# Kernel tuning notes

Measured on AMD Instinct MI355X. Metric: run time of the kernel, lower is better.

The kernel has to match this reference:

```python
import jax, jax.numpy as jnp
import numpy as np

N_LOC, C, A, H, X, STEPS = 500000, 128, 24, 256, 128, 4


def setup_inputs() -> dict:
    key = jax.random.key(0)
    ks = jax.random.split(key, 12)
    def rn(i, shape, scale=0.05):
        return jax.random.normal(ks[i], shape, dtype=jnp.float32) * scale
    return {
        "x": jax.random.normal(ks[0], (1, X), dtype=jnp.float32),
        "h0": jnp.zeros((1, H), jnp.float32),
        "memory_contents": rn(1, (N_LOC, C), 0.01),
        "memory_addresses": rn(2, (N_LOC, A), 0.1),
        "W_query": rn(3, (H, A + C)),
        "b_query": jnp.zeros((A + C,), jnp.float32),
        "u_sharpen": rn(4, (H,)),
        "b_sharpen": jnp.zeros((1,), jnp.float32),
        "W_erase": rn(5, (H, C)),
        "b_erase": jnp.zeros((C,), jnp.float32),
        "W_cand_h": rn(6, (H, C)),
        "W_cand_x": rn(7, (X, C)),
        "b_cand": jnp.zeros((C,), jnp.float32),
        "W_ih": rn(8, (X + C, 3 * H)),
        "W_hh": rn(9, (H, 3 * H)),
        "b_ih": jnp.zeros((3 * H,), jnp.float32),
        "b_hh": jnp.zeros((3 * H,), jnp.float32),
        "num_addressing_steps": STEPS,
    }


def _gru_cell(inp, h, W_ih, W_hh, b_ih, b_hh):
    # torch.nn.GRUCell semantics
    gi = inp @ W_ih + b_ih  # (1, 3H)
    gh = h @ W_hh + b_hh    # (1, 3H)
    i_r, i_z, i_n = jnp.split(gi, 3, axis=-1)
    h_r, h_z, h_n = jnp.split(gh, 3, axis=-1)
    r = jax.nn.sigmoid(i_r + h_r)
    z = jax.nn.sigmoid(i_z + h_z)
    n = jnp.tanh(i_n + r * h_n)
    return (1.0 - z) * n + z * h


def reference(x, h0, memory_contents, memory_addresses, W_query, b_query,
              u_sharpen, b_sharpen, W_erase, b_erase, W_cand_h, W_cand_x,
              b_cand, W_ih, W_hh, b_ih, b_hh, num_addressing_steps):
    h = h0                      # (1, H)
    mem = memory_contents       # (N, C)
    for _ in range(num_addressing_steps):
        # --- content-based addressing over full memory [addresses || contents] ---
        q = h @ W_query + b_query                              # (1, A+C)
        beta = jax.nn.softplus(h @ u_sharpen + b_sharpen) + 1.0  # (1,)
        sim = memory_addresses @ q[0, :A] + mem @ q[0, A:]     # (N,)
        w = jax.nn.softmax(beta[0] * sim)                      # (N,)
        # --- read ---
        content = (w @ mem)[None, :]                           # (1, C)
        # --- controller step ---
        h = _gru_cell(jnp.concatenate([x, content], axis=1), h, W_ih, W_hh, b_ih, b_hh)
        # --- write: erase + candidate ---
        erase = jax.nn.sigmoid(h @ W_erase + b_erase)          # (1, C)
        cand = jax.nn.relu(h @ W_cand_h + x @ W_cand_x + b_cand)  # (1, C)
        mem = mem * (1.0 - w[:, None] * erase) + w[:, None] * cand
    return h
```

## Files before the change

kernel.cpp:

```cpp
#include <hip/hip_runtime.h>
#include <hip/hip_bf16.h>

#define N_LOC 500000
#define C 128
#define A 24
#define AC 152
#define H 256
#define X 128
#define G3 768
#define GRID_BIG 1024

typedef unsigned short ushort_t;

__device__ __forceinline__ float sigmoidf_(float x) { return 1.0f / (1.0f + __expf(-x)); }

__device__ __forceinline__ ushort_t f2bf(float f) {
    unsigned u = __float_as_uint(f);
    u += 0x7FFFu + ((u >> 16) & 1u);
    return (ushort_t)(u >> 16);
}
__device__ __forceinline__ float bf2f(ushort_t s) {
    return __uint_as_float(((unsigned)s) << 16);
}

template <int NPREV, bool WRITE_E, bool CONVERT>
__global__ __launch_bounds__(256) void big_pass(
    const float* __restrict__ mem0, const float* __restrict__ addr,
    ushort_t* __restrict__ membf, ushort_t* __restrict__ addrbf,
    const float* __restrict__ qacc,
    const float* __restrict__ ehist,
    const float* __restrict__ chist,
    const float* __restrict__ ssum4,
    const float* __restrict__ earr,
    float* __restrict__ enew,
    float* __restrict__ part)
{
    const int lane = threadIdx.x & 31;
    const int rg   = threadIdx.x >> 5;

    const float4 qc = *(const float4*)(qacc + A + 4 * lane);
    float4 qa = make_float4(0.f, 0.f, 0.f, 0.f);
    if (lane < 6) qa = *(const float4*)(qacc + 4 * lane);
    float beta;
    { float t = qacc[AC]; beta = (t > 20.f ? t : log1pf(__expf(t))) + 1.0f; }

    constexpr int NP = (NPREV > 0) ? NPREV : 1;
    float4 er[NP], cd[NP];
    float inv_s[NP];
#pragma unroll
    for (int s = 0; s < NPREV; ++s) {
        float4 et = *(const float4*)(ehist + (s + 1) * C + 4 * lane);
        er[s].x = sigmoidf_(et.x); er[s].y = sigmoidf_(et.y);
        er[s].z = sigmoidf_(et.z); er[s].w = sigmoidf_(et.w);
        float4 ct = *(const float4*)(chist + (s + 1) * C + 4 * lane);
        cd[s].x = fmaxf(ct.x, 0.f); cd[s].y = fmaxf(ct.y, 0.f);
        cd[s].z = fmaxf(ct.z, 0.f); cd[s].w = fmaxf(ct.w, 0.f);
        inv_s[s] = 1.0f / ssum4[s + 1];
    }

    float4 acc = make_float4(0.f, 0.f, 0.f, 0.f);
    float sumloc = 0.f;
    const int stride = gridDim.x * 8;

    for (int i = blockIdx.x * 8 + rg; i < N_LOC; i += stride) {
        float4 m, a4 = make_float4(0.f, 0.f, 0.f, 0.f);
        if (CONVERT) {
            m = *(const float4*)(mem0 + (size_t)i * C + 4 * lane);
            ushort4 mu; mu.x = f2bf(m.x); mu.y = f2bf(m.y);
            mu.z = f2bf(m.z); mu.w = f2bf(m.w);
            *(ushort4*)(membf + (size_t)i * C + 4 * lane) = mu;
            if (lane < 6) {
                a4 = *(const float4*)(addr + (size_t)i * A + 4 * lane);
                ushort4 au; au.x = f2bf(a4.x); au.y = f2bf(a4.y);
                au.z = f2bf(a4.z); au.w = f2bf(a4.w);
                *(ushort4*)(addrbf + (size_t)i * A + 4 * lane) = au;
            }
        } else {
            ushort4 mu = *(const ushort4*)(membf + (size_t)i * C + 4 * lane);
            m = make_float4(bf2f(mu.x), bf2f(mu.y), bf2f(mu.z), bf2f(mu.w));
            if (lane < 6) {
                ushort4 au = *(const ushort4*)(addrbf + (size_t)i * A + 4 * lane);
                a4 = make_float4(bf2f(au.x), bf2f(au.y), bf2f(au.z), bf2f(au.w));
            }
        }

#pragma unroll
        for (int s = 0; s < NPREV; ++s) {
            float w = earr[s * N_LOC + i] * inv_s[s];
            m.x = m.x * (1.f - w * er[s].x) + w * cd[s].x;
            m.y = m.y * (1.f - w * er[s].y) + w * cd[s].y;
            m.z = m.z * (1.f - w * er[s].z) + w * cd[s].z;
            m.w = m.w * (1.f - w * er[s].w) + w * cd[s].w;
        }

        float s = m.x * qc.x + m.y * qc.y + m.z * qc.z + m.w * qc.w;
        s += a4.x * qa.x + a4.y * qa.y + a4.z * qa.z + a4.w * qa.w;
        s += __shfl_xor(s, 1);
        s += __shfl_xor(s, 2);
        s += __shfl_xor(s, 4);
        s += __shfl_xor(s, 8);
        s += __shfl_xor(s, 16);
        float ev = __expf(beta * s);
        if (WRITE_E && lane == 0) enew[i] = ev;
        if (lane == 0) sumloc += ev;
        acc.x += ev * m.x; acc.y += ev * m.y;
        acc.z += ev * m.z; acc.w += ev * m.w;
    }

    __shared__ float sc[8][C];
    __shared__ float ssum[256];
    *(float4*)(&sc[rg][4 * lane]) = acc;
    ssum[threadIdx.x] = sumloc;
    __syncthreads();
    if (threadIdx.x < C) {
        float v = 0.f;
#pragma unroll
        for (int g = 0; g < 8; ++g) v += sc[g][threadIdx.x];
        part[blockIdx.x * 132 + threadIdx.x] = v;
    }
    for (int off = 128; off > 0; off >>= 1) {
        if (threadIdx.x < off) ssum[threadIdx.x] += ssum[threadIdx.x + off];
        __syncthreads();
    }
    if (threadIdx.x == 0) part[blockIdx.x * 132 + C] = ssum[0];
}

__global__ __launch_bounds__(256) void reduce_part(
    const float* __restrict__ part, float* __restrict__ craw,
    float* __restrict__ ssum4, int step)
{
    const int j = blockIdx.x;
    float v = 0.f;
    for (int b = threadIdx.x; b < GRID_BIG; b += 256)
        v += part[b * 132 + j];
    __shared__ float sh[256];
    sh[threadIdx.x] = v;
    __syncthreads();
    for (int off = 128; off > 0; off >>= 1) {
        if (threadIdx.x < off) sh[threadIdx.x] += sh[threadIdx.x + off];
        __syncthreads();
    }
    if (threadIdx.x == 0) {
        craw[j] = sh[0];
        if (j == C) ssum4[step] = sh[0];
    }
}

__global__ __launch_bounds__(256) void prex(
    const float* __restrict__ x, const float* __restrict__ W_ih,
    const float* __restrict__ b_ih, const float* __restrict__ W_cx,
    float* __restrict__ gix, float* __restrict__ candx)
{
    const int tid = threadIdx.x;
    float a0 = 0.f, a1 = 0.f, a2 = 0.f, ac = 0.f;
    const int k0 = blockIdx.x * 8;
    for (int k = k0; k < k0 + 8; ++k) {
        float xk = x[k];
        const float* row = W_ih + (size_t)k * G3;
        a0 += xk * row[tid];
        a1 += xk * row[256 + tid];
        a2 += xk * row[512 + tid];
        if (tid < C) ac += xk * W_cx[k * C + tid];
    }
    const bool b0 = (blockIdx.x == 0);
    atomicAdd(gix + tid,        a0 + (b0 ? b_ih[tid] : 0.f));
    atomicAdd(gix + 256 + tid,  a1 + (b0 ? b_ih[256 + tid] : 0.f));
    atomicAdd(gix + 512 + tid,  a2 + (b0 ? b_ih[512 + tid] : 0.f));
    if (tid < C) atomicAdd(candx + tid, ac);
}

__global__ __launch_bounds__(256) void post(
    const float* __restrict__ h,
    const float* __restrict__ W_er, const float* __restrict__ b_er,
    const float* __restrict__ W_ch, const float* __restrict__ b_cd,
    const float* __restrict__ W_q,  const float* __restrict__ b_q,
    const float* __restrict__ u_sh, const float* __restrict__ b_sh,
    const float* __restrict__ candx,
    float* __restrict__ eslot, float* __restrict__ cslot,
    float* __restrict__ qacc)
{
    const int tid = threadIdx.x;
    float ae = 0.f, ac = 0.f, aq = 0.f, ab = 0.f;
    const int k0 = blockIdx.x * 16;
    for (int k = k0; k < k0 + 16; ++k) {
        float hk = h[k];
        if (tid < C)  { ae += hk * W_er[k * C + tid]; ac += hk * W_ch[k * C + tid]; }
        if (tid < AC)   aq += hk * W_q[k * AC + tid];
        if (tid == 255) ab += hk * u_sh[k];
    }
    const bool b0 = (blockIdx.x == 0);
    if (tid < C) {
        atomicAdd(eslot + tid, ae + (b0 ? b_er[tid] : 0.f));
        atomicAdd(cslot + tid, ac + (b0 ? (candx[tid] + b_cd[tid]) : 0.f));
    }
    if (tid < AC)   atomicAdd(qacc + tid, aq + (b0 ? b_q[tid] : 0.f));
    if (tid == 255) atomicAdd(qacc + AC, ab + (b0 ? b_sh[0] : 0.f));
}

__global__ __launch_bounds__(256) void gatesfin(
    const float* __restrict__ craw, const float* __restrict__ hprev,
    const float* __restrict__ W_ih, const float* __restrict__ W_hh,
    const float* __restrict__ b_hh, const float* __restrict__ gix,
    float* __restrict__ p2, float* __restrict__ hout,
    float* __restrict__ qacc, unsigned* __restrict__ counter)
{
    const int tid = threadIdx.x;
    const float inv = 1.0f / craw[C];
    float gi0 = 0.f, gi1 = 0.f, gi2 = 0.f, gh0 = 0.f, gh1 = 0.f, gh2 = 0.f;
    const int kc0 = blockIdx.x * 8;
    for (int k = kc0; k < kc0 + 8; ++k) {
        float ck = craw[k] * inv;
        const float* row = W_ih + (size_t)(X + k) * G3;
        gi0 += ck * row[tid]; gi1 += ck * row[256 + tid]; gi2 += ck * row[512 + tid];
    }
    const int kh0 = blockIdx.x * 16;
    for (int k = kh0; k < kh0 + 16; ++k) {
        float hk = hprev[k];
        const float* row = W_hh + (size_t)k * G3;
        gh0 += hk * row[tid]; gh1 += hk * row[256 + tid]; gh2 += hk * row[512 + tid];
    }
    const bool b0 = (blockIdx.x == 0);
    float* pb = p2 + blockIdx.x * 1536;
    pb[tid]        = gi0 + (b0 ? gix[tid] : 0.f);
    pb[256 + tid]  = gi1 + (b0 ? gix[256 + tid] : 0.f);
    pb[512 + tid]  = gi2 + (b0 ? gix[512 + tid] : 0.f);
    pb[768 + tid]  = gh0 + (b0 ? b_hh[tid] : 0.f);
    pb[1024 + tid] = gh1 + (b0 ? b_hh[256 + tid] : 0.f);
    pb[1280 + tid] = gh2 + (b0 ? b_hh[512 + tid] : 0.f);
    __threadfence();
    __syncthreads();
    __shared__ int lastBlk;
    if (tid == 0) lastBlk = (atomicAdd(counter, 1u) == 15u) ? 1 : 0;
    __syncthreads();
    if (!lastBlk) return;
    __threadfence();
    float ir = 0.f, iz = 0.f, in_ = 0.f, hr = 0.f, hz = 0.f, hn = 0.f;
    for (int b = 0; b < 16; ++b) {
        const float* q = p2 + b * 1536;
        ir += q[tid]; iz += q[256 + tid]; in_ += q[512 + tid];
        hr += q[768 + tid]; hz += q[1024 + tid]; hn += q[1280 + tid];
    }
    float r = sigmoidf_(ir + hr);
    float z = sigmoidf_(iz + hz);
    float n = tanhf(in_ + r * hn);
    hout[tid] = (1.f - z) * n + z * hprev[tid];
    if (tid < 160) qacc[tid] = 0.f;
    if (tid == 0) *counter = 0u;
}

extern "C" void kernel_launch(void* const* d_in, const int* in_sizes, int n_in,
                              void* d_out, int out_size, void* d_ws, size_t ws_size,
                              hipStream_t stream) {
    (void)in_sizes; (void)n_in; (void)out_size; (void)ws_size;
    const float* x    = (const float*)d_in[0];
    const float* h0   = (const float*)d_in[1];
    const float* mem0 = (const float*)d_in[2];
    const float* addr = (const float*)d_in[3];
    const float* W_q  = (const float*)d_in[4];
    const float* b_q  = (const float*)d_in[5];
    const float* u_sh = (const float*)d_in[6];
    const float* b_sh = (const float*)d_in[7];
    const float* W_er = (const float*)d_in[8];
    const float* b_er = (const float*)d_in[9];
    const float* W_ch = (const float*)d_in[10];
    const float* W_cx = (const float*)d_in[11];
    const float* b_cd = (const float*)d_in[12];
    const float* W_ih = (const float*)d_in[13];
    const float* W_hh = (const float*)d_in[14];
    const float* b_ih = (const float*)d_in[15];
    const float* b_hh = (const float*)d_in[16];
    float* hout = (float*)d_out;

    float*    e      = (float*)d_ws;
    ushort_t* membf  = (ushort_t*)(e + 3 * N_LOC);
    ushort_t* addrbf = membf + (size_t)N_LOC * C;
    float*    part   = (float*)(addrbf + (size_t)N_LOC * A);
    float*    S      = part + GRID_BIG * 132;
    float*    craw   = S;
    float*    qacc   = S + 144;
    float*    ehist  = S + 304;
    float*    chist  = S + 816;
    float*    gix    = S + 1328;
    float*    candx  = S + 2096;
    float*    ssum4  = S + 2224;
    unsigned* counter= (unsigned*)(S + 2232);
    float*    p2     = S + 2240;

    hipMemsetAsync(S, 0, 2240 * sizeof(float), stream);
    prex<<<16, 256, 0, stream>>>(x, W_ih, b_ih, W_cx, gix, candx);
    post<<<16, 256, 0, stream>>>(h0, W_er, b_er, W_ch, b_cd, W_q, b_q, u_sh, b_sh,
                                 candx, ehist, chist, qacc);
    big_pass<0, true, true><<<GRID_BIG, 256, 0, stream>>>(
        mem0, addr, membf, addrbf, qacc, ehist, chist, ssum4, e, e, part);
    reduce_part<<<129, 256, 0, stream>>>(part, craw, ssum4, 1);
    gatesfin<<<16, 256, 0, stream>>>(craw, h0, W_ih, W_hh, b_hh, gix, p2, hout,
                                     qacc, counter);
    post<<<16, 256, 0, stream>>>(hout, W_er, b_er, W_ch, b_cd, W_q, b_q, u_sh, b_sh,
                                 candx, ehist + C, chist + C, qacc);
    big_pass<1, true, false><<<GRID_BIG, 256, 0, stream>>>(
        mem0, addr, membf, addrbf, qacc, ehist, chist, ssum4, e, e + N_LOC, part);
    reduce_part<<<129, 256, 0, stream>>>(part, craw, ssum4, 2);
    gatesfin<<<16, 256, 0, stream>>>(craw, hout, W_ih, W_hh, b_hh, gix, p2, hout,
                                     qacc, counter);
    post<<<16, 256, 0, stream>>>(hout, W_er, b_er, W_ch, b_cd, W_q, b_q, u_sh, b_sh,
                                 candx, ehist + 2 * C, chist + 2 * C, qacc);
    big_pass<2, true, false><<<GRID_BIG, 256, 0, stream>>>(
        mem0, addr, membf, addrbf, qacc, ehist, chist, ssum4, e, e + 2 * N_LOC, part);
    reduce_part<<<129, 256, 0, stream>>>(part, craw, ssum4, 3);
    gatesfin<<<16, 256, 0, stream>>>(craw, hout, W_ih, W_hh, b_hh, gix, p2, hout,
                                     qacc, counter);
    post<<<16, 256, 0, stream>>>(hout, W_er, b_er, W_ch, b_cd, W_q, b_q, u_sh, b_sh,
                                 candx, ehist + 3 * C, chist + 3 * C, qacc);
    big_pass<3, false, false><<<GRID_BIG, 256, 0, stream>>>(
        mem0, addr, membf, addrbf, qacc, ehist, chist, ssum4, e, e, part);
    reduce_part<<<129, 256, 0, stream>>>(part, craw, ssum4, 4);
    gatesfin<<<16, 256, 0, stream>>>(craw, hout, W_ih, W_hh, b_hh, gix, p2, hout,
                                     qacc, counter);
}
```

Baseline: 749.1 us.

## Store memory snapshot in scaled FP8 and fuse step reduction, gates, and projections

The bf16 copy of the memory contents becomes an FP8 (e4m3) copy scaled by 64, with the scale folded into the query and candidate vectors. This halves the bytes each big pass reads per row. Separately, the reduce, gates and post kernels merge into one step_fin kernel using a transposed partial-sum layout, and prex plus the first post merge into init_k, which cuts kernel launches per step. The cost is much coarser precision for memory values, since FP8 keeps only three mantissa bits, which may break tolerance. The last block now also does the full 256-wide H projection serially.

```diff
diff --git a/kernel.cpp b/kernel.cpp
--- a/kernel.cpp
+++ b/kernel.cpp
@@ -1,5 +1,4 @@
 #include <hip/hip_runtime.h>
-#include <hip/hip_bf16.h>
 
 #define N_LOC 500000
 #define C 128
@@ -9,8 +8,12 @@
 #define X 128
 #define G3 768
 #define GRID_BIG 1024
+#define MSCALE 64.0f
+#define MINV 0.015625f
 
 typedef unsigned short ushort_t;
+typedef unsigned char uchar_t;
+typedef float floatx2 __attribute__((ext_vector_type(2)));
 
 __device__ __forceinline__ float sigmoidf_(float x) { return 1.0f / (1.0f + __expf(-x)); }
 
@@ -23,10 +26,60 @@
     return __uint_as_float(((unsigned)s) << 16);
 }
 
+#if defined(__has_builtin)
+#if __has_builtin(__builtin_amdgcn_cvt_pk_fp8_f32) && __has_builtin(__builtin_amdgcn_cvt_pk_f32_fp8)
+#define HAVE_HW_FP8 1
+#endif
+#endif
+
+__device__ __forceinline__ unsigned f2fp8_sw(float f) {
+    unsigned sgn = (__float_as_uint(f) >> 24) & 0x80u;
+    float af = fminf(fabsf(f), 448.0f);
+    unsigned q;
+    if (af < 0.015625f) {
+        q = (unsigned)__float2int_rn(af * 512.0f);
+    } else {
+        unsigned a = __float_as_uint(af);
+        a += 0x7FFFFu + ((a >> 20) & 1u);
+        unsigned e = (a >> 23) - 120u;
+        q = (e << 3) | ((a >> 20) & 7u);
+        if (q > 126u) q = 126u;
+    }
+    return q | sgn;
+}
+__device__ __forceinline__ float fp8d_sw(unsigned b) {
+    unsigned sgn = (b & 0x80u) << 24;
+    unsigned e = (b >> 3) & 15u;
+    unsigned m = b & 7u;
+    float fn = __uint_as_float(sgn | ((e + 120u) << 23) | (m << 20));
+    float fd = __uint_as_float(sgn | __float_as_uint((float)m * 0.001953125f));
+    return e ? fn : fd;
+}
+__device__ __forceinline__ unsigned pack_fp8x4(float4 m) {
+#ifdef HAVE_HW_FP8
+    int w = 0;
+    w = __builtin_amdgcn_cvt_pk_fp8_f32(m.x, m.y, w, false);
+    w = __builtin_amdgcn_cvt_pk_fp8_f32(m.z, m.w, w, true);
+    return (unsigned)w;
+#else
+    return f2fp8_sw(m.x) | (f2fp8_sw(m.y) << 8) | (f2fp8_sw(m.z) << 16) | (f2fp8_sw(m.w) << 24);
+#endif
+}
+__device__ __forceinline__ float4 unpack_fp8x4(unsigned w) {
+#ifdef HAVE_HW_FP8
+    floatx2 lo = __builtin_amdgcn_cvt_pk_f32_fp8((int)w, false);
+    floatx2 hi = __builtin_amdgcn_cvt_pk_f32_fp8((int)w, true);
+    return make_float4(lo[0], lo[1], hi[0], hi[1]);
+#else
+    return make_float4(fp8d_sw(w & 255u), fp8d_sw((w >> 8) & 255u),
+                       fp8d_sw((w >> 16) & 255u), fp8d_sw(w >> 24));
+#endif
+}
+
 template <int NPREV, bool WRITE_E, bool CONVERT>
 __global__ __launch_bounds__(256) void big_pass(
     const float* __restrict__ mem0, const float* __restrict__ addr,
-    ushort_t* __restrict__ membf, ushort_t* __restrict__ addrbf,
+    uchar_t* __restrict__ memq, ushort_t* __restrict__ addrbf,
     const float* __restrict__ qacc,
     const float* __restrict__ ehist,
     const float* __restrict__ chist,
@@ -38,7 +91,8 @@
     const int lane = threadIdx.x & 31;
     const int rg   = threadIdx.x >> 5;
 
-    const float4 qc = *(const float4*)(qacc + A + 4 * lane);
+    float4 qc = *(const float4*)(qacc + A + 4 * lane);
+    qc.x *= MINV; qc.y *= MINV; qc.z *= MINV; qc.w *= MINV;
     float4 qa = make_float4(0.f, 0.f, 0.f, 0.f);
     if (lane < 6) qa = *(const float4*)(qacc + 4 * lane);
     float beta;
@@ -53,8 +107,10 @@
         er[s].x = sigmoidf_(et.x); er[s].y = sigmoidf_(et.y);
         er[s].z = sigmoidf_(et.z); er[s].w = sigmoidf_(et.w);
         float4 ct = *(const float4*)(chist + (s + 1) * C + 4 * lane);
-        cd[s].x = fmaxf(ct.x, 0.f); cd[s].y = fmaxf(ct.y, 0.f);
-        cd[s].z = fmaxf(ct.z, 0.f); cd[s].w = fmaxf(ct.w, 0.f);
+        cd[s].x = fmaxf(ct.x, 0.f) * MSCALE;
+        cd[s].y = fmaxf(ct.y, 0.f) * MSCALE;
+        cd[s].z = fmaxf(ct.z, 0.f) * MSCALE;
+        cd[s].w = fmaxf(ct.w, 0.f) * MSCALE;
         inv_s[s] = 1.0f / ssum4[s + 1];
     }
 
@@ -65,10 +121,10 @@
     for (int i = blockIdx.x * 8 + rg; i < N_LOC; i += stride) {
         float4 m, a4 = make_float4(0.f, 0.f, 0.f, 0.f);
         if (CONVERT) {
-            m = *(const float4*)(mem0 + (size_t)i * C + 4 * lane);
-            ushort4 mu; mu.x = f2bf(m.x); mu.y = f2bf(m.y);
-            mu.z = f2bf(m.z); mu.w = f2bf(m.w);
-            *(ushort4*)(membf + (size_t)i * C + 4 * lane) = mu;
+            float4 mf = *(const float4*)(mem0 + (size_t)i * C + 4 * lane);
+            m.x = mf.x * MSCALE; m.y = mf.y * MSCALE;
+            m.z = mf.z * MSCALE; m.w = mf.w * MSCALE;
+            *(unsigned*)(memq + (size_t)i * C + 4 * lane) = pack_fp8x4(m);
             if (lane < 6) {
                 a4 = *(const float4*)(addr + (size_t)i * A + 4 * lane);
                 ushort4 au; au.x = f2bf(a4.x); au.y = f2bf(a4.y);
@@ -76,8 +132,8 @@
                 *(ushort4*)(addrbf + (size_t)i * A + 4 * lane) = au;
             }
         } else {
-            ushort4 mu = *(const ushort4*)(membf + (size_t)i * C + 4 * lane);
-            m = make_float4(bf2f(mu.x), bf2f(mu.y), bf2f(mu.z), bf2f(mu.w));
+            unsigned mw = *(const unsigned*)(memq + (size_t)i * C + 4 * lane);
+            m = unpack_fp8x4(mw);
             if (lane < 6) {
                 ushort4 au = *(const ushort4*)(addrbf + (size_t)i * A + 4 * lane);
                 a4 = make_float4(bf2f(au.x), bf2f(au.y), bf2f(au.z), bf2f(au.w));
@@ -93,14 +149,14 @@
             m.w = m.w * (1.f - w * er[s].w) + w * cd[s].w;
         }
 
-        float s = m.x * qc.x + m.y * qc.y + m.z * qc.z + m.w * qc.w;
-        s += a4.x * qa.x + a4.y * qa.y + a4.z * qa.z + a4.w * qa.w;
-        s += __shfl_xor(s, 1);
-        s += __shfl_xor(s, 2);
-        s += __shfl_xor(s, 4);
-        s += __shfl_xor(s, 8);
-        s += __shfl_xor(s, 16);
-        float ev = __expf(beta * s);
+        float sv = m.x * qc.x + m.y * qc.y + m.z * qc.z + m.w * qc.w;
+        sv += a4.x * qa.x + a4.y * qa.y + a4.z * qa.z + a4.w * qa.w;
+        sv += __shfl_xor(sv, 1);
+        sv += __shfl_xor(sv, 2);
+        sv += __shfl_xor(sv, 4);
+        sv += __shfl_xor(sv, 8);
+        sv += __shfl_xor(sv, 16);
+        float ev = __expf(beta * sv);
         if (WRITE_E && lane == 0) enew[i] = ev;
         if (lane == 0) sumloc += ev;
         acc.x += ev * m.x; acc.y += ev * m.y;
@@ -116,117 +172,122 @@
         float v = 0.f;
 #pragma unroll
         for (int g = 0; g < 8; ++g) v += sc[g][threadIdx.x];
-        part[blockIdx.x * 132 + threadIdx.x] = v;
+        part[(size_t)threadIdx.x * GRID_BIG + blockIdx.x] = v;
     }
     for (int off = 128; off > 0; off >>= 1) {
         if (threadIdx.x < off) ssum[threadIdx.x] += ssum[threadIdx.x + off];
         __syncthreads();
     }
-    if (threadIdx.x == 0) part[blockIdx.x * 132 + C] = ssum[0];
-}
-
-__global__ __launch_bounds__(256) void reduce_part(
-    const float* __restrict__ part, float* __restrict__ craw,
-    float* __restrict__ ssum4, int step)
-{
-    const int j = blockIdx.x;
-    float v = 0.f;
-    for (int b = threadIdx.x; b < GRID_BIG; b += 256)
-        v += part[b * 132 + j];
-    __shared__ float sh[256];
-    sh[threadIdx.x] = v;
-    __syncthreads();
-    for (int off = 128; off > 0; off >>= 1) {
-        if (threadIdx.x < off) sh[threadIdx.x] += sh[threadIdx.x + off];
-        __syncthreads();
-    }
-    if (threadIdx.x == 0) {
-        craw[j] = sh[0];
-        if (j == C) ssum4[step] = sh[0];
-    }
-}
-
-__global__ __launch_bounds__(256) void prex(
-    const float* __restrict__ x, const float* __restrict__ W_ih,
-    const float* __restrict__ b_ih, const float* __restrict__ W_cx,
-    float* __restrict__ gix, float* __restrict__ candx)
+    if (threadIdx.x == 0) part[(size_t)C * GRID_BIG + blockIdx.x] = ssum[0];
+}
+
+__global__ __launch_bounds__(256) void init_k(
+    const float* __restrict__ x, const float* __restrict__ h0,
+    const float* __restrict__ W_ih, const float* __restrict__ b_ih,
+    const float* __restrict__ W_cx,
+    const float* __restrict__ W_er, const float* __restrict__ b_er,
+    const float* __restrict__ W_ch, const float* __restrict__ b_cd,
+    const float* __restrict__ W_q,  const float* __restrict__ b_q,
+    const float* __restrict__ u_sh, const float* __restrict__ b_sh,
+    float* __restrict__ gix, float* __restrict__ candx,
+    float* __restrict__ eslot, float* __restrict__ cslot,
+    float* __restrict__ qacc)
 {
     const int tid = threadIdx.x;
-    float a0 = 0.f, a1 = 0.f, a2 = 0.f, ac = 0.f;
-    const int k0 = blockIdx.x * 8;
-    for (int k = k0; k < k0 + 8; ++k) {
-        float xk = x[k];
-        const float* row = W_ih + (size_t)k * G3;
-        a0 += xk * row[tid];
-        a1 += xk * row[256 + tid];
-        a2 += xk * row[512 + tid];
-        if (tid < C) ac += xk * W_cx[k * C + tid];
-    }
     const bool b0 = (blockIdx.x == 0);
-    atomicAdd(gix + tid,        a0 + (b0 ? b_ih[tid] : 0.f));
-    atomicAdd(gix + 256 + tid,  a1 + (b0 ? b_ih[256 + tid] : 0.f));
-    atomicAdd(gix + 512 + tid,  a2 + (b0 ? b_ih[512 + tid] : 0.f));
-    if (tid < C) atomicAdd(candx + tid, ac);
-}
-
-__global__ __launch_bounds__(256) void post(
-    const float* __restrict__ h,
+    {
+        float a0 = 0.f, a1 = 0.f, a2 = 0.f, ac = 0.f;
+        const int k0 = blockIdx.x * 8;
+        for (int k = k0; k < k0 + 8; ++k) {
+            float xk = x[k];
+            const float* row = W_ih + (size_t)k * G3;
+            a0 += xk * row[tid];
+            a1 += xk * row[256 + tid];
+            a2 += xk * row[512 + tid];
+            if (tid < C) ac += xk * W_cx[k * C + tid];
+        }
+        atomicAdd(gix + tid,        a0 + (b0 ? b_ih[tid] : 0.f));
+        atomicAdd(gix + 256 + tid,  a1 + (b0 ? b_ih[256 + tid] : 0.f));
+        atomicAdd(gix + 512 + tid,  a2 + (b0 ? b_ih[512 + tid] : 0.f));
+        if (tid < C) atomicAdd(candx + tid, ac);
+    }
+    {
+        float ae = 0.f, ac2 = 0.f, aq = 0.f, ab = 0.f;
+        const int k0 = blockIdx.x * 16;
+        for (int k = k0; k < k0 + 16; ++k) {
+            float hk = h0[k];
+            if (tid < C)  { ae += hk * W_er[k * C + tid]; ac2 += hk * W_ch[k * C + tid]; }
+            if (tid < AC)   aq += hk * W_q[k * AC + tid];
+            if (tid == 255) ab += hk * u_sh[k];
+        }
+        if (tid < C) {
+            atomicAdd(eslot + tid, ae + (b0 ? b_er[tid] : 0.f));
+            atomicAdd(cslot + tid, ac2 + (b0 ? b_cd[tid] : 0.f));
+        }
+        if (tid < AC)   atomicAdd(qacc + tid, aq + (b0 ? b_q[tid] : 0.f));
+        if (tid == 255) atomicAdd(qacc + AC, ab + (b0 ? b_sh[0] : 0.f));
+    }
+}
+
+__global__ __launch_bounds__(256) void step_fin(
+    const float* __restrict__ part, float* __restrict__ craw,
+    float* __restrict__ ssum4, int step,
+    const float* __restrict__ hprev,
+    const float* __restrict__ W_ih, const float* __restrict__ W_hh,
+    const float* __restrict__ b_hh, const float* __restrict__ gix,
+    float* __restrict__ p2, float* __restrict__ hout,
     const float* __restrict__ W_er, const float* __restrict__ b_er,
     const float* __restrict__ W_ch, const float* __restrict__ b_cd,
     const float* __restrict__ W_q,  const float* __restrict__ b_q,
     const float* __restrict__ u_sh, const float* __restrict__ b_sh,
     const float* __restrict__ candx,
     float* __restrict__ eslot, float* __restrict__ cslot,
-    float* __restrict__ qacc)
+    float* __restrict__ qnext,
+    unsigned* __restrict__ counter, int do_post)
 {
     const int tid = threadIdx.x;
-    float ae = 0.f, ac = 0.f, aq = 0.f, ab = 0.f;
-    const int k0 = blockIdx.x * 16;
-    for (int k = k0; k < k0 + 16; ++k) {
-        float hk = h[k];
-        if (tid < C)  { ae += hk * W_er[k * C + tid]; ac += hk * W_ch[k * C + tid]; }
-        if (tid < AC)   aq += hk * W_q[k * AC + tid];
-        if (tid == 255) ab += hk * u_sh[k];
-    }
-    const bool b0 = (blockIdx.x == 0);
-    if (tid < C) {
-        atomicAdd(eslot + tid, ae + (b0 ? b_er[tid] : 0.f));
-        atomicAdd(cslot + tid, ac + (b0 ? (candx[tid] + b_cd[tid]) : 0.f));
-    }
-    if (tid < AC)   atomicAdd(qacc + tid, aq + (b0 ? b_q[tid] : 0.f));
-    if (tid == 255) atomicAdd(qacc + AC, ab + (b0 ? b_sh[0] : 0.f));
-}
-
-__global__ __launch_bounds__(256) void gatesfin(
-    const float* __restrict__ craw, const float* __restrict__ hprev,
-    const float* __restrict__ W_ih, const float* __restrict__ W_hh,
-    const float* __restrict__ b_hh, const float* __restrict__ gix,
-    float* __restrict__ p2, float* __restrict__ hout,
-    float* __restrict__ qacc, unsigned* __restrict__ counter)
-{
-    const int tid = threadIdx.x;
-    const float inv = 1.0f / craw[C];
-    float gi0 = 0.f, gi1 = 0.f, gi2 = 0.f, gh0 = 0.f, gh1 = 0.f, gh2 = 0.f;
-    const int kc0 = blockIdx.x * 8;
-    for (int k = kc0; k < kc0 + 8; ++k) {
-        float ck = craw[k] * inv;
-        const float* row = W_ih + (size_t)(X + k) * G3;
-        gi0 += ck * row[tid]; gi1 += ck * row[256 + tid]; gi2 += ck * row[512 + tid];
-    }
-    const int kh0 = blockIdx.x * 16;
-    for (int k = kh0; k < kh0 + 16; ++k) {
-        float hk = hprev[k];
-        const float* row = W_hh + (size_t)k * G3;
-        gh0 += hk * row[tid]; gh1 += hk * row[256 + tid]; gh2 += hk * row[512 + tid];
-    }
-    const bool b0 = (blockIdx.x == 0);
-    float* pb = p2 + blockIdx.x * 1536;
-    pb[tid]        = gi0 + (b0 ? gix[tid] : 0.f);
-    pb[256 + tid]  = gi1 + (b0 ? gix[256 + tid] : 0.f);
-    pb[512 + tid]  = gi2 + (b0 ? gix[512 + tid] : 0.f);
-    pb[768 + tid]  = gh0 + (b0 ? b_hh[tid] : 0.f);
-    pb[1024 + tid] = gh1 + (b0 ? b_hh[256 + tid] : 0.f);
-    pb[1280 + tid] = gh2 + (b0 ? b_hh[512 + tid] : 0.f);
+    __shared__ float scol[4];
+    __shared__ float myc[9];
+
+    for (int j = blockIdx.x; j < C + 1; j += 16) {
+        float v = 0.f;
+        for (int b = tid; b < GRID_BIG; b += 256) v += part[(size_t)j * GRID_BIG + b];
+        v += __shfl_xor(v, 1);  v += __shfl_xor(v, 2);  v += __shfl_xor(v, 4);
+        v += __shfl_xor(v, 8);  v += __shfl_xor(v, 16); v += __shfl_xor(v, 32);
+        if ((tid & 63) == 0) scol[tid >> 6] = v;
+        __syncthreads();
+        if (tid == 0) {
+            float sv = scol[0] + scol[1] + scol[2] + scol[3];
+            if (j < C) myc[(j - blockIdx.x) >> 4] = sv * MINV;
+            else       { craw[C] = sv; ssum4[step] = sv; }
+        }
+        __syncthreads();
+    }
+
+    {
+        float gi0 = 0.f, gi1 = 0.f, gi2 = 0.f;
+        int idx = 0;
+        for (int j = blockIdx.x; j < C; j += 16, ++idx) {
+            float ck = myc[idx];
+            const float* row = W_ih + (size_t)(X + j) * G3;
+            gi0 += ck * row[tid]; gi1 += ck * row[256 + tid]; gi2 += ck * row[512 + tid];
+        }
+        float gh0 = 0.f, gh1 = 0.f, gh2 = 0.f;
+        const int kh0 = blockIdx.x * 16;
+        for (int k = kh0; k < kh0 + 16; ++k) {
+            float hk = hprev[k];
+            const float* row = W_hh + (size_t)k * G3;
+            gh0 += hk * row[tid]; gh1 += hk * row[256 + tid]; gh2 += hk * row[512 + tid];
+        }
+        float* pb = p2 + blockIdx.x * 1536;
+        pb[tid]        = gi0;
+        pb[256 + tid]  = gi1;
+        pb[512 + tid]  = gi2;
+        pb[768 + tid]  = gh0;
+        pb[1024 + tid] = gh1;
+        pb[1280 + tid] = gh2;
+    }
+
     __threadfence();
     __syncthreads();
     __shared__ int lastBlk;
@@ -234,18 +295,43 @@
     __syncthreads();
     if (!lastBlk) return;
     __threadfence();
-    float ir = 0.f, iz = 0.f, in_ = 0.f, hr = 0.f, hz = 0.f, hn = 0.f;
+
+    float giA = 0.f, giB = 0.f, giC = 0.f, ghA = 0.f, ghB = 0.f, ghC = 0.f;
     for (int b = 0; b < 16; ++b) {
         const float* q = p2 + b * 1536;
-        ir += q[tid]; iz += q[256 + tid]; in_ += q[512 + tid];
-        hr += q[768 + tid]; hz += q[1024 + tid]; hn += q[1280 + tid];
-    }
+        giA += q[tid];       giB += q[256 + tid];  giC += q[512 + tid];
+        ghA += q[768 + tid]; ghB += q[1024 + tid]; ghC += q[1280 + tid];
+    }
+    const float inv = 1.0f / craw[C];
+    float ir  = giA * inv + gix[tid];
+    float iz  = giB * inv + gix[256 + tid];
+    float in_ = giC * inv + gix[512 + tid];
+    float hr  = ghA + b_hh[tid];
+    float hz  = ghB + b_hh[256 + tid];
+    float hn  = ghC + b_hh[512 + tid];
     float r = sigmoidf_(ir + hr);
     float z = sigmoidf_(iz + hz);
     float n = tanhf(in_ + r * hn);
-    hout[tid] = (1.f - z) * n + z * hprev[tid];
-    if (tid < 160) qacc[tid] = 0.f;
-    if (tid == 0) *counter = 0u;
+    float h = (1.f - z) * n + z * hprev[tid];
+    hout[tid] = h;
+    if (!do_post) return;
+
+    __shared__ float hsh[H];
+    hsh[tid] = h;
+    __syncthreads();
+    float ae = 0.f, ac = 0.f, aq = 0.f, ab = 0.f;
+    for (int k = 0; k < H; ++k) {
+        float hk = hsh[k];
+        if (tid < C)  { ae += hk * W_er[k * C + tid]; ac += hk * W_ch[k * C + tid]; }
+        if (tid < AC)   aq += hk * W_q[k * AC + tid];
+        if (tid == 255) ab += hk * u_sh[k];
+    }
+    if (tid < C) {
+        eslot[tid] = ae + b_er[tid];
+        cslot[tid] = ac + candx[tid] + b_cd[tid];
+    }
+    if (tid < AC)   qnext[tid] = aq + b_q[tid];
+    if (tid == 255) qnext[AC]  = ab + b_sh[0];
 }
 
 extern "C" void kernel_launch(void* const* d_in, const int* in_sizes, int n_in,
@@ -272,48 +358,41 @@
     float* hout = (float*)d_out;
 
     float*    e      = (float*)d_ws;
-    ushort_t* membf  = (ushort_t*)(e + 3 * N_LOC);
-    ushort_t* addrbf = membf + (size_t)N_LOC * C;
+    uchar_t*  memq   = (uchar_t*)(e + 3 * N_LOC);
+    ushort_t* addrbf = (ushort_t*)(memq + (size_t)N_LOC * C);
     float*    part   = (float*)(addrbf + (size_t)N_LOC * A);
-    float*    S      = part + GRID_BIG * 132;
-    float*    craw   = S;
-    float*    qacc   = S + 144;
-    float*    ehist  = S + 304;
-    float*    chist  = S + 816;
-    float*    gix    = S + 1328;
-    float*    candx  = S + 2096;
-    float*    ssum4  = S + 2224;
-    unsigned* counter= (unsigned*)(S + 2232);
-    float*    p2     = S + 2240;
-
-    hipMemsetAsync(S, 0, 2240 * sizeof(float), stream);
-    prex<<<16, 256, 0, stream>>>(x, W_ih, b_ih, W_cx, gix, candx);
-    post<<<16, 256, 0, stream>>>(h0, W_er, b_er, W_ch, b_cd, W_q, b_q, u_sh, b_sh,
-                                 candx, ehist, chist, qacc);
+    float*    p2     = part + 132 * GRID_BIG;
+    float*    craw   = p2 + 16 * 1536;
+    float*    S0     = craw + 132;
+    float*    gix    = S0;
+    float*    candx  = S0 + 768;
+    float*    qaccs  = S0 + 896;
+    float*    ehist  = S0 + 1696;
+    float*    chist  = S0 + 2336;
+    float*    ssum4  = S0 + 2976;
+    unsigned* cnt    = (unsigned*)(S0 + 2984);
+
+    hipMemsetAsync(S0, 0, 3000 * sizeof(float), stream);
+    init_k<<<16, 256, 0, stream>>>(x, h0, W_ih, b_ih, W_cx, W_er, b_er, W_ch, b_cd,
+                                   W_q, b_q, u_sh, b_sh, gix, candx, ehist, chist, qaccs);
     big_pass<0, true, true><<<GRID_BIG, 256, 0, stream>>>(
-        mem0, addr, membf, addrbf, qacc, ehist, chist, ssum4, e, e, part);
-    reduce_part<<<129, 256, 0, stream>>>(part, craw, ssum4, 1);
-    gatesfin<<<16, 256, 0, stream>>>(craw, h0, W_ih, W_hh, b_hh, gix, p2, hout,
-                                     qacc, counter);
-    post<<<16, 256, 0, stream>>>(hout, W_er, b_er, W_ch, b_cd, W_q, b_q, u_sh, b_sh,
-                                 candx, ehist + C, chist + C, qacc);
+        mem0, addr, memq, addrbf, qaccs, ehist, chist, ssum4, e, e, part);
+    step_fin<<<16, 256, 0, stream>>>(part, craw, ssum4, 1, h0, W_ih, W_hh, b_hh, gix,
+        p2, hout, W_er, b_er, W_ch, b_cd, W_q, b_q, u_sh, b_sh, candx,
+        ehist + C, chist + C, qaccs + 160, cnt + 0, 1);
     big_pass<1, true, false><<<GRID_BIG, 256, 0, stream>>>(
-        mem0, addr, membf, addrbf, qacc, ehist, chist, ssum4, e, e + N_LOC, part);
-    reduce_part<<<129, 256, 0, stream>>>(part, craw, ssum4, 2);
-    gatesfin<<<16, 256, 0, stream>>>(craw, hout, W_ih, W_hh, b_hh, gix, p2, hout,
-                                     qacc, counter);
-    post<<<16, 256, 0, stream>>>(hout, W_er, b_er, W_ch, b_cd, W_q, b_q, u_sh, b_sh,
-                                 candx, ehist + 2 * C, chist + 2 * C, qacc);
+        mem0, addr, memq, addrbf, qaccs + 160, ehist, chist, ssum4, e, e + N_LOC, part);
+    step_fin<<<16, 256, 0, stream>>>(part, craw, ssum4, 2, hout, W_ih, W_hh, b_hh, gix,
+        p2, hout, W_er, b_er, W_ch, b_cd, W_q, b_q, u_sh, b_sh, candx,
+        ehist + 2 * C, chist + 2 * C, qaccs + 320, cnt + 1, 1);
     big_pass<2, true, false><<<GRID_BIG, 256, 0, stream>>>(
-        mem0, addr, membf, addrbf, qacc, ehist, chist, ssum4, e, e + 2 * N_LOC, part);
-    reduce_part<<<129, 256, 0, stream>>>(part, craw, ssum4, 3);
-    gatesfin<<<16, 256, 0, stream>>>(craw, hout, W_ih, W_hh, b_hh, gix, p2, hout,
-                                     qacc, counter);
-    post<<<16, 256, 0, stream>>>(hout, W_er, b_er, W_ch, b_cd, W_q, b_q, u_sh, b_sh,
-                                 candx, ehist + 3 * C, chist + 3 * C, qacc);
+        mem0, addr, memq, addrbf, qaccs + 320, ehist, chist, ssum4, e, e + 2 * N_LOC, part);
+    step_fin<<<16, 256, 0, stream>>>(part, craw, ssum4, 3, hout, W_ih, W_hh, b_hh, gix,
+        p2, hout, W_er, b_er, W_ch, b_cd, W_q, b_q, u_sh, b_sh, candx,
+        ehist + 3 * C, chist + 3 * C, qaccs + 480, cnt + 2, 1);
     big_pass<3, false, false><<<GRID_BIG, 256, 0, stream>>>(
-        mem0, addr, membf, addrbf, qacc, ehist, chist, ssum4, e, e, part);
-    reduce_part<<<129, 256, 0, stream>>>(part, craw, ssum4, 4);
-    gatesfin<<<16, 256, 0, stream>>>(craw, hout, W_ih, W_hh, b_hh, gix, p2, hout,
-                                     qacc, counter);
-}
+        mem0, addr, memq, addrbf, qaccs + 480, ehist, chist, ssum4, e, e, part);
+    step_fin<<<16, 256, 0, stream>>>(part, craw, ssum4, 4, hout, W_ih, W_hh, b_hh, gix,
+        p2, hout, W_er, b_er, W_ch, b_cd, W_q, b_q, u_sh, b_sh, candx,
+        ehist + 4 * C, chist + 4 * C, qaccs + 640, cnt + 3, 0);
+}
```

Result: slower. 1.222 ms (+63.2%).
